# Kernel tuning notes

Hardware: AMD Instinct MI355X
Metric: run time of the kernel (lower is better)

Reference implementation:

```python
import jax, jax.numpy as jnp
import numpy as np

NBX = 24  # nb_x_patches
NBY = 24  # nb_y_patches
B, H, D = 8, 12, 64
L = NBX * NBY + 1  # 577 (grid tokens + 1 CLS token from the pad)
EPS = 1e-08


def _toeplitz_mask(topological_params):
    # topological_params: [H, 4*NBX*NBY]
    gi = jnp.arange(NBX)
    gj = jnp.arange(NBY)
    # relative 2D displacement index, flattened over (i, j, i', j')
    dist_index = ((gi[:, None, None, None] - gi[None, None, :, None] + NBX) * 2 * NBY
                  + gj[None, :, None, None] - gj[None, None, None, :] + NBY)
    dist_index = dist_index.reshape(-1)
    m = jnp.take(topological_params, dist_index, axis=1)
    m = m.reshape(topological_params.shape[0], NBX * NBY, NBX * NBY)  # [H, L-1, L-1]
    # pad CLS row and column with 1.0
    m = jnp.pad(m, [[0, 0], [1, 0], [1, 0]], constant_values=1.0)  # [H, L, L]
    return m[None]  # [1, H, L, L]


def setup_inputs() -> dict:
    key = jax.random.key(0)
    k1, k2, k3, k4 = jax.random.split(key, 4)
    return {
        'query': jax.random.normal(k1, (B, L, H, D), dtype=jnp.float32),
        'key': jax.random.normal(k2, (B, L, H, D), dtype=jnp.float32),
        'value': jax.random.normal(k3, (B, L, H, D), dtype=jnp.float32),
        'topological_params': jax.random.normal(k4, (H, 4 * NBX * NBY), dtype=jnp.float32),
    }


def reference(query, key, value, topological_params):
    depth = query.shape[-1]
    q = query / jnp.sqrt(jnp.asarray(depth, query.dtype))
    # relu feature map (kernel_type == 'relu')
    q = jax.nn.relu(q) + EPS
    k = jax.nn.relu(key) + EPS
    attn = jnp.einsum('bqhd,bkhd->bhqk', q, k)  # [B, H, L, L]
    top_mask = _toeplitz_mask(topological_params)  # [1, H, L, L]
    attn = attn * jnp.abs(top_mask) + EPS
    attn = attn / jnp.sum(attn, axis=-1, keepdims=True)  # kernelized normalization (no softmax)
    return jnp.einsum('bhqk,bkhd->bqhd', attn, value)
```

## Files before the change

### kernel.cpp

```cpp
#include <hip/hip_runtime.h>


#define Lq 577
#define NH 12
#define NB 8
#define DD 64
#define PAR 2304
#define EPSf 1e-8f

#define VT_OFF 7090176ull
#define MM_OFF 14954496ull

#define PK_BLOCKS  1731
#define PVT_BLOCKS 960
#define PM_BLOCKS  2316

typedef __attribute__((ext_vector_type(4))) float f32x4;
typedef __attribute__((ext_vector_type(8))) short s16x8;

__device__ __forceinline__ float bflo(unsigned int u) {
    return __builtin_bit_cast(float, u << 16);
}
__device__ __forceinline__ float bfhi(unsigned int u) {
    return __builtin_bit_cast(float, u & 0xffff0000u);
}
__device__ __forceinline__ unsigned int f2bf(float f) {
    unsigned int x = __builtin_bit_cast(unsigned int, f);
    return (x + 0x7fffu + ((x >> 16) & 1u)) >> 16;
}
__device__ __forceinline__ int imin(int a, int b) { return a < b ? a : b; }

__device__ __forceinline__ void gload_lds16(const unsigned short* g, unsigned short* l) {
    __builtin_amdgcn_global_load_lds(
        (const __attribute__((address_space(1))) unsigned int*)g,
        (__attribute__((address_space(3))) unsigned int*)l, 16, 0, 0);
}

__device__ __forceinline__ bool probe_f32(const void* Qg) {
    float x = fabsf(((const float*)Qg)[threadIdx.x]);
    unsigned long long hit = __ballot(x > 2.44140625e-4f && x < 64.0f);
    unsigned long long act = __ballot(1);
    return 2 * __popcll(hit) >= __popcll(act);
}

template <bool F32>
__device__ __forceinline__ void load8f(const void* G, size_t eidx, float* o) {
    if constexpr (F32) {
        const float* p = (const float*)G + eidx;
        float4 a = *(const float4*)p;
        float4 b = *(const float4*)(p + 4);
        o[0] = a.x; o[1] = a.y; o[2] = a.z; o[3] = a.w;
        o[4] = b.x; o[5] = b.y; o[6] = b.z; o[7] = b.w;
    } else {
        const unsigned short* p = (const unsigned short*)G + eidx;
        uint4 a = *(const uint4*)p;
        unsigned int u[4] = {a.x, a.y, a.z, a.w};
#pragma unroll
        for (int j = 0; j < 4; ++j) {
            o[2 * j]     = bflo(u[j]);
            o[2 * j + 1] = bfhi(u[j]);
        }
    }
}

template <bool F32>
__device__ void prep_all_body(const void* __restrict__ Kg,
                              const void* __restrict__ Vg,
                              const void* __restrict__ Tg,
                              unsigned short* __restrict__ Kp,
                              unsigned short* __restrict__ Vt,
                              unsigned short* __restrict__ Mm,
                              unsigned short* s) {
    const int bid = blockIdx.x;
    const int t   = threadIdx.x;

    if (bid < PK_BLOCKS) {
        size_t i8 = ((size_t)bid * 256 + t) * 8;
        float f[8];
        load8f<F32>(Kg, i8, f);
        unsigned int o[4];
#pragma unroll
        for (int j = 0; j < 4; ++j) {
            unsigned int lo = f2bf(fmaxf(f[2 * j], 0.0f) + EPSf);
            unsigned int hi = f2bf(fmaxf(f[2 * j + 1], 0.0f) + EPSf);
            o[j] = lo | (hi << 16);
        }
        *(uint4*)(Kp + i8) = make_uint4(o[0], o[1], o[2], o[3]);

    } else if (bid < PK_BLOCKS + PVT_BLOCKS) {
        int r  = bid - PK_BLOCKS;
        int kt = r % 10; r /= 10;
        int h  = r % NH;
        int b  = r / NH;
        {
            int kl  = t >> 2;
            int dch = (t & 3) * 16;
            int k   = kt * 64 + kl;
            unsigned int pk[8] = {};
            if (k <= 576) {
                float f[16];
                size_t base = ((size_t)((b * Lq + k) * NH + h)) * DD + dch;
                load8f<F32>(Vg, base, f);
                load8f<F32>(Vg, base + 8, f + 8);
#pragma unroll
                for (int j = 0; j < 8; ++j)
                    pk[j] = f2bf(f[2 * j]) | (f2bf(f[2 * j + 1]) << 16);
            }
#pragma unroll
            for (int j = 0; j < 8; ++j)
                *(unsigned int*)&s[kl * 72 + dch + 2 * j] = pk[j];
        }
        __syncthreads();
        {
            int d   = t >> 2;
            int kch = (t & 3) * 16;
            unsigned int o[8];
#pragma unroll
            for (int j = 0; j < 8; ++j) {
                unsigned short v0 = s[(kch + 2 * j) * 72 + d];
                unsigned short v1 = s[(kch + 2 * j + 1) * 72 + d];
                o[j] = (unsigned int)v0 | ((unsigned int)v1 << 16);
            }
            size_t base = ((size_t)((b * NH + h) * 64 + d)) * 640 + kt * 64 + kch;
            *(uint4*)(Vt + base)     = make_uint4(o[0], o[1], o[2], o[3]);
            *(uint4*)(Vt + base + 8) = make_uint4(o[4], o[5], o[6], o[7]);
        }

    } else {
        int r  = bid - (PK_BLOCKS + PVT_BLOCKS);
        int h  = r / 193;
        int qb = (r % 193) * 3;
        if (t < 240) {
            int q = qb + t / 80;
            if (q < Lq) {
                int k0 = (t % 80) * 8;
                int cq = 0;
                if (q > 0) {
                    int qq = q - 1;
                    int qi = (qq * 2731) >> 16;
                    cq = qq + 24 * qi + 1176;
                }
                unsigned int o[4];
#pragma unroll
                for (int j = 0; j < 4; ++j) {
                    unsigned int hv[2];
#pragma unroll
                    for (int e = 0; e < 2; ++e) {
                        int k = k0 + 2 * j + e;
                        float m;
                        if (k > 576) m = 0.0f;
                        else if (k == 0 || q == 0) m = 1.0f;
                        else {
                            int kk = k - 1;
                            int ki = (kk * 2731) >> 16;
                            int idx = cq - (kk + 24 * ki);
                            float pv = F32 ? ((const float*)Tg)[h * PAR + idx]
                                           : bflo((unsigned int)((const unsigned short*)Tg)[h * PAR + idx]);
                            m = fabsf(pv);
                            m = (m == m) ? m : 0.0f;
                        }
                        hv[e] = f2bf(m);
                    }
                    o[j] = hv[0] | (hv[1] << 16);
                }
                *(uint4*)(Mm + (size_t)(h * Lq + q) * 640 + k0) = make_uint4(o[0], o[1], o[2], o[3]);
            }
        }
    }
}
__global__ __launch_bounds__(256)
void prep_all(const void* __restrict__ Qg, const void* __restrict__ Kg,
              const void* __restrict__ Vg, const void* __restrict__ Tg,
              unsigned short* __restrict__ Kp, unsigned short* __restrict__ Vt,
              unsigned short* __restrict__ Mm) {
    __shared__ __align__(16) unsigned short s[64 * 72];
    if (probe_f32(Qg)) prep_all_body<true>(Kg, Vg, Tg, Kp, Vt, Mm, s);
    else               prep_all_body<false>(Kg, Vg, Tg, Kp, Vt, Mm, s);
}

template <bool F32>
__device__ void attn_body(const void* __restrict__ Qg,
                          const unsigned short* __restrict__ Kp,
                          const unsigned short* __restrict__ Vt,
                          const unsigned short* __restrict__ Mm,
                          void* __restrict__ Og,
                          unsigned short* s_k, unsigned short* s_vt,
                          unsigned short* s_p_all) {
    const int tid  = threadIdx.x;
    const int w    = tid >> 6;
    const int lane = tid & 63;
    const int g    = lane >> 4;
    const int lm   = lane & 15;

    const int bid = blockIdx.x;
    const int qt  = bid / 96;
    const int bh  = bid - qt * 96;
    const int h   = bh % NH;
    const int b   = bh / NH;

    unsigned short* s_pw = s_p_all + w * 16 * 64;
    const int q0w = qt * 64 + w * 16;

    const int q  = q0w + lm;
    const int qc = imin(q, Lq - 1);
    s16x8 a_q[2];
    {
        size_t rbase = ((size_t)((b * Lq + qc) * NH + h)) * DD;
#pragma unroll
        for (int ds = 0; ds < 2; ++ds) {
            float f[8];
            load8f<F32>(Qg, rbase + ds * 32 + g * 8, f);
            s16x8 a;
#pragma unroll
            for (int j = 0; j < 8; ++j) {
                float v = fmaf(fmaxf(f[j], 0.0f), 0.125f, EPSf);
                a[j] = (short)f2bf(v);
            }
            a_q[ds] = a;
        }
    }

    const int r8 = lane >> 3;
    const int c8 = lane & 7;
    const int xr = (c8 ^ r8) * 8;

    const unsigned short* KpBH = Kp + (size_t)b * (Lq * NH * DD) + h * DD;
    const unsigned short* VtL0 = Vt + ((size_t)(b * NH + h) * 64 + (w * 16 + r8)) * 640 + xr;
    const unsigned short* VtL1 = VtL0 + 8 * 640;
    const unsigned short* MmQ  = Mm + (size_t)h * (Lq * 640) + (size_t)qc * 640 + g * 4;

    f32x4 o_acc[4] = {};
    float rs = 0.0f;
    const int x7 = lm & 7;

    auto stageKV = [&](int kb, int buf) {
        unsigned short* skb = s_k  + buf * 4096 + (w * 16) * 64;
        unsigned short* svb = s_vt + buf * 4096 + (w * 16) * 64;
        int krr = kb + w * 16 + r8;
        int kr0 = imin(krr, Lq - 1);
        int kr1 = imin(krr + 8, Lq - 1);
        gload_lds16(KpBH + (size_t)kr0 * (NH * DD) + xr, skb);
        gload_lds16(KpBH + (size_t)kr1 * (NH * DD) + xr, skb + 8 * 64);
        gload_lds16(VtL0 + kb, svb);
        gload_lds16(VtL1 + kb, svb + 8 * 64);
    };

    stageKV(0, 0);
    __syncthreads();

    for (int t = 0; t < 10; ++t) {
        const int kb  = t * 64;
        const int buf = t & 1;

        uint2 mu[4];
#pragma unroll
        for (int cf = 0; cf < 4; ++cf)
            mu[cf] = *(const uint2*)(MmQ + kb + cf * 16);

        if (t < 9) stageKV(kb + 64, buf ^ 1);

        const unsigned short* skB = s_k  + buf * 4096;
        const unsigned short* svB = s_vt + buf * 4096;

        f32x4 sf[4];
#pragma unroll
        for (int cf = 0; cf < 4; ++cf) {
            const unsigned short* skr = skB + (cf * 16 + lm) * 64;
            int co = (g ^ x7) * 8;
            s16x8 kf0 = *(const s16x8*)(skr + co);
            s16x8 kf1 = *(const s16x8*)(skr + (co ^ 32));
            f32x4 acc = {};
            acc = __builtin_amdgcn_mfma_f32_16x16x32_bf16(kf0, a_q[0], acc, 0, 0, 0);
            acc = __builtin_amdgcn_mfma_f32_16x16x32_bf16(kf1, a_q[1], acc, 0, 0, 0);
            sf[cf] = acc;
        }

#pragma unroll
        for (int cf = 0; cf < 4; ++cf) {
            float m0 = bflo(mu[cf].x), m1 = bfhi(mu[cf].x);
            float m2 = bflo(mu[cf].y), m3 = bfhi(mu[cf].y);
            float p0 = fmaf(fmaxf(sf[cf][0], 0.0f), m0, EPSf);
            float p1 = fmaf(fmaxf(sf[cf][1], 0.0f), m1, EPSf);
            float p2 = fmaf(fmaxf(sf[cf][2], 0.0f), m2, EPSf);
            float p3 = fmaf(fmaxf(sf[cf][3], 0.0f), m3, EPSf);
            rs += (p0 + p1) + (p2 + p3);
            unsigned int d0 = f2bf(p0) | (f2bf(p1) << 16);
            unsigned int d1 = f2bf(p2) | (f2bf(p3) << 16);
            int pc = (((cf * 2 + (g >> 1)) ^ x7) << 3) + ((g & 1) << 2);
            *(uint2*)&s_pw[lm * 64 + pc] = make_uint2(d0, d1);
        }

#pragma unroll
        for (int ks = 0; ks < 2; ++ks) {
            s16x8 pa = *(const s16x8*)&s_pw[lm * 64 + (((ks * 4 + g) ^ x7) << 3)];
#pragma unroll
            for (int df = 0; df < 4; ++df) {
                const unsigned short* svr = svB + (df * 16 + lm) * 64;
                s16x8 vb = *(const s16x8*)(svr + (((ks * 4 + g) ^ x7) << 3));
                o_acc[df] = __builtin_amdgcn_mfma_f32_16x16x32_bf16(pa, vb, o_acc[df], 0, 0, 0);
            }
        }

        if (t < 9) __syncthreads();
    }

    float tot = rs;
    tot += __shfl_xor(tot, 16, 64);
    tot += __shfl_xor(tot, 32, 64);
    float inv = (tot > 0.0f) ? 1.0f / tot : 0.0f;

#pragma unroll
    for (int r = 0; r < 4; ++r) {
        int   qrow  = q0w + g * 4 + r;
        float inv_r = __shfl(inv, g * 4 + r, 64);
        if (qrow < Lq) {
            size_t base = ((size_t)((b * Lq + qrow) * NH + h)) * DD;
#pragma unroll
            for (int df = 0; df < 4; ++df) {
                float val = o_acc[df][r] * inv_r;
                if constexpr (F32)
                    ((float*)Og)[base + df * 16 + lm] = val;
                else
                    ((unsigned short*)Og)[base + df * 16 + lm] = (unsigned short)f2bf(val);
            }
        }
    }
}

__global__ __launch_bounds__(256, 4)
void fused_topo_attn(const void* __restrict__ Qg,
                     const unsigned short* __restrict__ Kp,
                     const unsigned short* __restrict__ Vt,
                     const unsigned short* __restrict__ Mm,
                     void* __restrict__ Og) {
    __shared__ __align__(16) unsigned short s_k[2 * 64 * 64];
    __shared__ __align__(16) unsigned short s_vt[2 * 64 * 64];
    __shared__ __align__(16) unsigned short s_p[4 * 16 * 64];

    if (probe_f32(Qg)) attn_body<true>(Qg, Kp, Vt, Mm, Og, s_k, s_vt, s_p);
    else               attn_body<false>(Qg, Kp, Vt, Mm, Og, s_k, s_vt, s_p);
}

extern "C" void kernel_launch(void* const* d_in, const int* in_sizes, int n_in,
                              void* d_out, int out_size, void* d_ws, size_t ws_size,
                              hipStream_t stream) {
    (void)in_sizes; (void)n_in; (void)out_size; (void)ws_size;
    unsigned short* Kp = (unsigned short*)d_ws;
    unsigned short* Vt = (unsigned short*)((char*)d_ws + VT_OFF);
    unsigned short* Mm = (unsigned short*)((char*)d_ws + MM_OFF);

    prep_all<<<PK_BLOCKS + PVT_BLOCKS + PM_BLOCKS, 256, 0, stream>>>(
        d_in[0], d_in[1], d_in[2], d_in[3], Kp, Vt, Mm);
    fused_topo_attn<<<960, 256, 0, stream>>>(d_in[0], Kp, Vt, Mm, d_out);
}
```

Before: 124.8 us.

## Fuse K relu/bf16 conversion into attention kernel and remap block order by head

```diff
diff --git a/kernel.cpp b/kernel.cpp
--- a/kernel.cpp
+++ b/kernel.cpp
@@ -8,10 +8,8 @@
 #define PAR 2304
 #define EPSf 1e-8f
 
-#define VT_OFF 7090176ull
-#define MM_OFF 14954496ull
-
-#define PK_BLOCKS  1731
+#define MM_OFF 7864320ull
+
 #define PVT_BLOCKS 960
 #define PM_BLOCKS  2316
 
@@ -64,31 +62,16 @@
 }
 
 template <bool F32>
-__device__ void prep_all_body(const void* __restrict__ Kg,
-                              const void* __restrict__ Vg,
+__device__ void prep_all_body(const void* __restrict__ Vg,
                               const void* __restrict__ Tg,
-                              unsigned short* __restrict__ Kp,
                               unsigned short* __restrict__ Vt,
                               unsigned short* __restrict__ Mm,
                               unsigned short* s) {
     const int bid = blockIdx.x;
     const int t   = threadIdx.x;
 
-    if (bid < PK_BLOCKS) {
-        size_t i8 = ((size_t)bid * 256 + t) * 8;
-        float f[8];
-        load8f<F32>(Kg, i8, f);
-        unsigned int o[4];
-#pragma unroll
-        for (int j = 0; j < 4; ++j) {
-            unsigned int lo = f2bf(fmaxf(f[2 * j], 0.0f) + EPSf);
-            unsigned int hi = f2bf(fmaxf(f[2 * j + 1], 0.0f) + EPSf);
-            o[j] = lo | (hi << 16);
-        }
-        *(uint4*)(Kp + i8) = make_uint4(o[0], o[1], o[2], o[3]);
-
-    } else if (bid < PK_BLOCKS + PVT_BLOCKS) {
-        int r  = bid - PK_BLOCKS;
+    if (bid < PVT_BLOCKS) {
+        int r  = bid;
         int kt = r % 10; r /= 10;
         int h  = r % NH;
         int b  = r / NH;
@@ -127,7 +110,7 @@
         }
 
     } else {
-        int r  = bid - (PK_BLOCKS + PVT_BLOCKS);
+        int r  = bid - PVT_BLOCKS;
         int h  = r / 193;
         int qb = (r % 193) * 3;
         if (t < 240) {
@@ -169,18 +152,17 @@
     }
 }
 __global__ __launch_bounds__(256)
-void prep_all(const void* __restrict__ Qg, const void* __restrict__ Kg,
-              const void* __restrict__ Vg, const void* __restrict__ Tg,
-              unsigned short* __restrict__ Kp, unsigned short* __restrict__ Vt,
-              unsigned short* __restrict__ Mm) {
+void prep_all(const void* __restrict__ Qg, const void* __restrict__ Vg,
+              const void* __restrict__ Tg,
+              unsigned short* __restrict__ Vt, unsigned short* __restrict__ Mm) {
     __shared__ __align__(16) unsigned short s[64 * 72];
-    if (probe_f32(Qg)) prep_all_body<true>(Kg, Vg, Tg, Kp, Vt, Mm, s);
-    else               prep_all_body<false>(Kg, Vg, Tg, Kp, Vt, Mm, s);
+    if (probe_f32(Qg)) prep_all_body<true>(Vg, Tg, Vt, Mm, s);
+    else               prep_all_body<false>(Vg, Tg, Vt, Mm, s);
 }
 
 template <bool F32>
 __device__ void attn_body(const void* __restrict__ Qg,
-                          const unsigned short* __restrict__ Kp,
+                          const void* __restrict__ Kg,
                           const unsigned short* __restrict__ Vt,
                           const unsigned short* __restrict__ Mm,
                           void* __restrict__ Og,
@@ -192,11 +174,12 @@
     const int g    = lane >> 4;
     const int lm   = lane & 15;
 
-    const int bid = blockIdx.x;
-    const int qt  = bid / 96;
-    const int bh  = bid - qt * 96;
-    const int h   = bh % NH;
-    const int b   = bh / NH;
+    const int bid  = blockIdx.x;
+    const int slot = (bid & 7) * 120 + (bid >> 3);
+    const int h    = slot / 80;
+    const int rem  = slot - h * 80;
+    const int b    = rem / 10;
+    const int qt   = rem - b * 10;
 
     unsigned short* s_pw = s_p_all + w * 16 * 64;
     const int q0w = qt * 64 + w * 16;
@@ -223,8 +206,9 @@
     const int r8 = lane >> 3;
     const int c8 = lane & 7;
     const int xr = (c8 ^ r8) * 8;
-
-    const unsigned short* KpBH = Kp + (size_t)b * (Lq * NH * DD) + h * DD;
+    const int rl = lane >> 2;
+    const int cc = lane & 3;
+
     const unsigned short* VtL0 = Vt + ((size_t)(b * NH + h) * 64 + (w * 16 + r8)) * 640 + xr;
     const unsigned short* VtL1 = VtL0 + 8 * 640;
     const unsigned short* MmQ  = Mm + (size_t)h * (Lq * 640) + (size_t)qc * 640 + g * 4;
@@ -233,19 +217,38 @@
     float rs = 0.0f;
     const int x7 = lm & 7;
 
-    auto stageKV = [&](int kb, int buf) {
-        unsigned short* skb = s_k  + buf * 4096 + (w * 16) * 64;
+    auto stageV = [&](int kb, int buf) {
         unsigned short* svb = s_vt + buf * 4096 + (w * 16) * 64;
-        int krr = kb + w * 16 + r8;
-        int kr0 = imin(krr, Lq - 1);
-        int kr1 = imin(krr + 8, Lq - 1);
-        gload_lds16(KpBH + (size_t)kr0 * (NH * DD) + xr, skb);
-        gload_lds16(KpBH + (size_t)kr1 * (NH * DD) + xr, skb + 8 * 64);
         gload_lds16(VtL0 + kb, svb);
         gload_lds16(VtL1 + kb, svb + 8 * 64);
     };
-
-    stageKV(0, 0);
+    auto loadK = [&](int kbn, float* f) {
+        int kcl = imin(kbn + w * 16 + rl, Lq - 1);
+        size_t base = ((size_t)((b * Lq + kcl) * NH + h)) * DD + cc * 16;
+        load8f<F32>(Kg, base, f);
+        load8f<F32>(Kg, base + 8, f + 8);
+    };
+    auto writeK = [&](int buf, const float* f) {
+        unsigned short* skb = s_k + buf * 4096;
+        const int R  = w * 16 + rl;
+        const int r7 = R & 7;
+        unsigned int o[8];
+#pragma unroll
+        for (int j = 0; j < 8; ++j) {
+            unsigned int lo = f2bf(fmaxf(f[2 * j], 0.0f) + EPSf);
+            unsigned int hi = f2bf(fmaxf(f[2 * j + 1], 0.0f) + EPSf);
+            o[j] = lo | (hi << 16);
+        }
+        *(uint4*)(skb + R * 64 + (((2 * cc) ^ r7) << 3))     = make_uint4(o[0], o[1], o[2], o[3]);
+        *(uint4*)(skb + R * 64 + (((2 * cc + 1) ^ r7) << 3)) = make_uint4(o[4], o[5], o[6], o[7]);
+    };
+
+    {
+        float k0r[16];
+        loadK(0, k0r);
+        stageV(0, 0);
+        writeK(0, k0r);
+    }
     __syncthreads();
 
     for (int t = 0; t < 10; ++t) {
@@ -257,7 +260,11 @@
         for (int cf = 0; cf < 4; ++cf)
             mu[cf] = *(const uint2*)(MmQ + kb + cf * 16);
 
-        if (t < 9) stageKV(kb + 64, buf ^ 1);
+        float kn[16];
+        if (t < 9) {
+            loadK(kb + 64, kn);
+            stageV(kb + 64, buf ^ 1);
+        }
 
         const unsigned short* skB = s_k  + buf * 4096;
         const unsigned short* svB = s_vt + buf * 4096;
@@ -301,7 +308,10 @@
             }
         }
 
-        if (t < 9) __syncthreads();
+        if (t < 9) {
+            writeK(buf ^ 1, kn);
+            __syncthreads();
+        }
     }
 
     float tot = rs;
@@ -329,7 +339,7 @@
 
 __global__ __launch_bounds__(256, 4)
 void fused_topo_attn(const void* __restrict__ Qg,
-                     const unsigned short* __restrict__ Kp,
+                     const void* __restrict__ Kg,
                      const unsigned short* __restrict__ Vt,
                      const unsigned short* __restrict__ Mm,
                      void* __restrict__ Og) {
@@ -337,19 +347,18 @@
     __shared__ __align__(16) unsigned short s_vt[2 * 64 * 64];
     __shared__ __align__(16) unsigned short s_p[4 * 16 * 64];
 
-    if (probe_f32(Qg)) attn_body<true>(Qg, Kp, Vt, Mm, Og, s_k, s_vt, s_p);
-    else               attn_body<false>(Qg, Kp, Vt, Mm, Og, s_k, s_vt, s_p);
+    if (probe_f32(Qg)) attn_body<true>(Qg, Kg, Vt, Mm, Og, s_k, s_vt, s_p);
+    else               attn_body<false>(Qg, Kg, Vt, Mm, Og, s_k, s_vt, s_p);
 }
 
 extern "C" void kernel_launch(void* const* d_in, const int* in_sizes, int n_in,
                               void* d_out, int out_size, void* d_ws, size_t ws_size,
                               hipStream_t stream) {
     (void)in_sizes; (void)n_in; (void)out_size; (void)ws_size;
-    unsigned short* Kp = (unsigned short*)d_ws;
-    unsigned short* Vt = (unsigned short*)((char*)d_ws + VT_OFF);
+    unsigned short* Vt = (unsigned short*)d_ws;
     unsigned short* Mm = (unsigned short*)((char*)d_ws + MM_OFF);
 
-    prep_all<<<PK_BLOCKS + PVT_BLOCKS + PM_BLOCKS, 256, 0, stream>>>(
-        d_in[0], d_in[1], d_in[2], d_in[3], Kp, Vt, Mm);
-    fused_topo_attn<<<960, 256, 0, stream>>>(d_in[0], Kp, Vt, Mm, d_out);
-}
+    prep_all<<<PVT_BLOCKS + PM_BLOCKS, 256, 0, stream>>>(
+        d_in[0], d_in[2], d_in[3], Vt, Mm);
+    fused_topo_attn<<<960, 256, 0, stream>>>(d_in[0], d_in[1], Vt, Mm, d_out);
+}
```

New measurement: 130.5 us. 4.6% more time.
